# Performance work log

Measured on AMD Instinct MI355X. Metric: run time of the kernel, lower is better.

The kernel has to match this reference:

```python
import jax, jax.numpy as jnp
import numpy as np

MARGIN = 0.5
N_CLASSES = 100

def setup_inputs() -> dict:
    key = jax.random.key(0)
    k1, k2 = jax.random.split(key)
    n, d = 8192, 128
    inputs = jax.random.normal(k1, (n, d), dtype=jnp.float32)
    targets = jax.random.randint(k2, (n,), 0, N_CLASSES, dtype=jnp.int64)
    return {"inputs": inputs, "targets": targets}

def reference(inputs, targets):
    # pairwise squared euclidean distances: [n, n]
    sq = jnp.sum(inputs * inputs, axis=1)  # [n]
    dist = sq[:, None] + sq[None, :] - 2.0 * (inputs @ inputs.T)
    dist = jnp.maximum(dist, 0.0)
    # positive mask: same label (diagonal included, matching original)
    mask = targets[:, None] == targets[None, :]  # [n, n] bool
    big = jnp.float32(1e30)
    dist_ap = jnp.max(jnp.where(mask, dist, -big), axis=1)  # hardest positive per row
    dist_an = jnp.min(jnp.where(mask, big, dist), axis=1)   # hardest negative per row
    loss = jnp.sum(jax.nn.relu(dist_ap - dist_an + MARGIN))
    return loss
```

## Files before the change

kernel.cpp:

```cpp
#include <hip/hip_runtime.h>
#include <hip/hip_bf16.h>

#define D 128
#define MARGIN 0.5f
#define NSPLIT 16
#define NCHUNK 32

typedef __attribute__((ext_vector_type(8))) short bf16x8;
typedef __attribute__((ext_vector_type(4))) float f32x4;

__global__ void prep_kernel(const float* __restrict__ x,
                            float* __restrict__ sq,
                            unsigned* __restrict__ ap,
                            unsigned* __restrict__ an,
                            __hip_bfloat16* __restrict__ xb,
                            float* __restrict__ out, int n) {
    int tid = threadIdx.x;
    int row = blockIdx.x * 4 + (tid >> 6);
    int lane = tid & 63;
    const float2* xr = (const float2*)(x + (size_t)row * D);
    float2 v = xr[lane];
    __hip_bfloat162 b2;
    b2.x = __float2bfloat16(v.x);
    b2.y = __float2bfloat16(v.y);
    ((__hip_bfloat162*)(xb + (size_t)row * D))[lane] = b2;
    float s = v.x * v.x + v.y * v.y;
    #pragma unroll
    for (int o = 32; o > 0; o >>= 1) s += __shfl_xor(s, o, 64);
    if (lane == 0) {
        sq[row] = s;
        ap[row] = 0u;
        an[row] = 0x7F800000u;
    }
    if (blockIdx.x == 0 && tid == 0) *out = 0.0f;
}

__launch_bounds__(256, 2)
__global__ void gram_kernel(const __hip_bfloat16* __restrict__ xb,
                            const float* __restrict__ sq,
                            const int* __restrict__ tgt,
                            unsigned* __restrict__ ap,
                            unsigned* __restrict__ an, int n) {
    const int tid  = threadIdx.x;
    const int wid  = tid >> 6;
    const int lane = tid & 63;
    const int quad = lane >> 4;
    const int l    = lane & 15;
    const int gw     = blockIdx.x * 4 + wid;
    const int istrip = gw >> 4;
    const int jsplit = gw & 15;
    const int i0 = istrip * 64;
    const int j0 = jsplit * (16 * NCHUNK);

    bf16x8 afrag[4][4];
    {
        const __hip_bfloat16* abase = xb + (size_t)(i0 + l) * D + quad * 8;
        #pragma unroll
        for (int mt = 0; mt < 4; ++mt)
            #pragma unroll
            for (int ks = 0; ks < 4; ++ks)
                afrag[mt][ks] = *(const bf16x8*)(abase + (size_t)mt * 16 * D + ks * 32);
    }

    int li[4][4];
    #pragma unroll
    for (int mt = 0; mt < 4; ++mt)
        #pragma unroll
        for (int reg = 0; reg < 4; ++reg)
            li[mt][reg] = tgt[i0 + mt * 16 + quad * 4 + reg];

    float lap[16], lan[16];
    #pragma unroll
    for (int k = 0; k < 16; ++k) { lap[k] = -1e30f; lan[k] = 1e30f; }

    const __hip_bfloat16* bbase = xb + (size_t)(j0 + l) * D + quad * 8;

    bf16x8 bf[2][4];
    float  sj[2];
    int    tj[2];

    #define LOADB(buf, c)                                                   \
        do {                                                                \
            const __hip_bfloat16* p_ = bbase + (size_t)(c) * 16 * D;        \
            bf[buf][0] = *(const bf16x8*)(p_);                              \
            bf[buf][1] = *(const bf16x8*)(p_ + 32);                         \
            bf[buf][2] = *(const bf16x8*)(p_ + 64);                         \
            bf[buf][3] = *(const bf16x8*)(p_ + 96);                         \
            sj[buf] = sq[j0 + (c) * 16 + l];                                \
            tj[buf] = tgt[j0 + (c) * 16 + l];                               \
        } while (0)

    #define COMPUTE(buf)                                                    \
        do {                                                                \
            f32x4 acc[4];                                                   \
            _Pragma("unroll")                                               \
            for (int mt = 0; mt < 4; ++mt) acc[mt] = (f32x4){0.f,0.f,0.f,0.f}; \
            _Pragma("unroll")                                               \
            for (int ks = 0; ks < 4; ++ks)                                  \
                _Pragma("unroll")                                           \
                for (int mt = 0; mt < 4; ++mt)                              \
                    acc[mt] = __builtin_amdgcn_mfma_f32_16x16x32_bf16(      \
                        afrag[mt][ks], bf[buf][ks], acc[mt], 0, 0, 0);      \
            float sjc = sj[buf]; int tjc = tj[buf];                         \
            _Pragma("unroll")                                               \
            for (int mt = 0; mt < 4; ++mt)                                  \
                _Pragma("unroll")                                           \
                for (int reg = 0; reg < 4; ++reg) {                         \
                    float t = fmaf(-2.0f, acc[mt][reg], sjc);               \
                    bool same = (li[mt][reg] == tjc);                       \
                    lap[mt*4+reg] = fmaxf(lap[mt*4+reg], same ? t : -1e30f);\
                    lan[mt*4+reg] = fminf(lan[mt*4+reg], same ? 1e30f : t); \
                }                                                           \
        } while (0)

    LOADB(0, 0);
    for (int c = 0; c < NCHUNK; c += 2) {
        LOADB(1, c + 1);
        COMPUTE(0);
        if (c < NCHUNK - 2) LOADB(0, c + 2);
        COMPUTE(1);
    }
    #undef LOADB
    #undef COMPUTE

    #pragma unroll
    for (int mt = 0; mt < 4; ++mt)
        #pragma unroll
        for (int reg = 0; reg < 4; ++reg) {
            float p = lap[mt*4+reg], q = lan[mt*4+reg];
            #pragma unroll
            for (int o = 1; o < 16; o <<= 1) {
                p = fmaxf(p, __shfl_xor(p, o, 64));
                q = fminf(q, __shfl_xor(q, o, 64));
            }
            if (l == mt * 4 + reg) {
                int gi = i0 + mt * 16 + quad * 4 + reg;
                float s = sq[gi];
                atomicMax(&ap[gi], __float_as_uint(fmaxf(s + p, 0.0f)));
                atomicMin(&an[gi], __float_as_uint(fmaxf(s + q, 0.0f)));
            }
        }
}

__global__ void final_kernel(const unsigned* __restrict__ ap,
                             const unsigned* __restrict__ an,
                             float* __restrict__ out, int n) {
    int i = blockIdx.x * blockDim.x + threadIdx.x;
    float v = 0.f;
    if (i < n) {
        float p = __uint_as_float(ap[i]);
        float q = __uint_as_float(an[i]);
        v = fmaxf(p - q + MARGIN, 0.0f);
    }
    #pragma unroll
    for (int o = 32; o > 0; o >>= 1) v += __shfl_xor(v, o, 64);
    __shared__ float ws[4];
    int lane = threadIdx.x & 63, w = threadIdx.x >> 6;
    if (lane == 0) ws[w] = v;
    __syncthreads();
    if (threadIdx.x == 0) atomicAdd(out, ws[0] + ws[1] + ws[2] + ws[3]);
}

extern "C" void kernel_launch(void* const* d_in, const int* in_sizes, int n_in,
                              void* d_out, int out_size, void* d_ws, size_t ws_size,
                              hipStream_t stream) {
    const float* x   = (const float*)d_in[0];
    const int*   tgt = (const int*)d_in[1];
    float* out = (float*)d_out;
    const int n = in_sizes[1];

    float*          sq = (float*)d_ws;
    unsigned*       ap = (unsigned*)((char*)d_ws + (size_t)n * 4);
    unsigned*       an = ap + n;
    __hip_bfloat16* xb = (__hip_bfloat16*)((char*)d_ws + (size_t)n * 12);

    prep_kernel<<<n / 4, 256, 0, stream>>>(x, sq, ap, an, xb, out, n);
    gram_kernel<<<(n / 64) * NSPLIT / 4, 256, 0, stream>>>(xb, sq, tgt, ap, an, n);
    final_kernel<<<n / 256, 256, 0, stream>>>(ap, an, out, n);
}
```

Baseline: 103.1 us.

## Stage shared B tiles in LDS with swizzle and double buffering

Before, each wave streamed its own B fragments straight from global memory, covering 64 rows over a private j range. Now a block of 4 waves covers 128 rows and shares each 64-row B tile, staged in swizzled double-buffered LDS with register prefetch. This raises B reuse across waves and lowers global traffic, and each wave now holds 32 rows, so register pressure falls enough to allow 4 blocks per CU. The cost is a __syncthreads per tile and LDS read traffic, and each wave does fewer MFMAs per B fragment.

```diff
diff --git a/kernel.cpp b/kernel.cpp
--- a/kernel.cpp
+++ b/kernel.cpp
@@ -4,7 +4,6 @@
 #define D 128
 #define MARGIN 0.5f
 #define NSPLIT 16
-#define NCHUNK 32
 
 typedef __attribute__((ext_vector_type(8))) short bf16x8;
 typedef __attribute__((ext_vector_type(4))) float f32x4;
@@ -35,106 +34,126 @@
     if (blockIdx.x == 0 && tid == 0) *out = 0.0f;
 }
 
-__launch_bounds__(256, 2)
+__launch_bounds__(256, 4)
 __global__ void gram_kernel(const __hip_bfloat16* __restrict__ xb,
                             const float* __restrict__ sq,
                             const int* __restrict__ tgt,
                             unsigned* __restrict__ ap,
                             unsigned* __restrict__ an, int n) {
+    __shared__ __align__(16) __hip_bfloat16 Bs[2][64 * D];
+
     const int tid  = threadIdx.x;
     const int wid  = tid >> 6;
     const int lane = tid & 63;
     const int quad = lane >> 4;
     const int l    = lane & 15;
-    const int gw     = blockIdx.x * 4 + wid;
-    const int istrip = gw >> 4;
-    const int jsplit = gw & 15;
-    const int i0 = istrip * 64;
-    const int j0 = jsplit * (16 * NCHUNK);
-
-    bf16x8 afrag[4][4];
+    const int i0   = blockIdx.x * 128;
+    const int jspan = n / NSPLIT;
+    const int njit  = jspan / 64;
+    const int j0    = blockIdx.y * jspan;
+    const int rowbase = i0 + wid * 32;
+
+    bf16x8 afrag[2][4];
     {
-        const __hip_bfloat16* abase = xb + (size_t)(i0 + l) * D + quad * 8;
-        #pragma unroll
-        for (int mt = 0; mt < 4; ++mt)
+        const __hip_bfloat16* abase = xb + (size_t)(rowbase + l) * D + quad * 8;
+        #pragma unroll
+        for (int mt = 0; mt < 2; ++mt)
             #pragma unroll
             for (int ks = 0; ks < 4; ++ks)
                 afrag[mt][ks] = *(const bf16x8*)(abase + (size_t)mt * 16 * D + ks * 32);
     }
 
-    int li[4][4];
-    #pragma unroll
-    for (int mt = 0; mt < 4; ++mt)
+    int li[2][4];
+    #pragma unroll
+    for (int mt = 0; mt < 2; ++mt)
         #pragma unroll
         for (int reg = 0; reg < 4; ++reg)
-            li[mt][reg] = tgt[i0 + mt * 16 + quad * 4 + reg];
-
-    float lap[16], lan[16];
-    #pragma unroll
-    for (int k = 0; k < 16; ++k) { lap[k] = -1e30f; lan[k] = 1e30f; }
-
-    const __hip_bfloat16* bbase = xb + (size_t)(j0 + l) * D + quad * 8;
-
-    bf16x8 bf[2][4];
-    float  sj[2];
-    int    tj[2];
-
-    #define LOADB(buf, c)                                                   \
-        do {                                                                \
-            const __hip_bfloat16* p_ = bbase + (size_t)(c) * 16 * D;        \
-            bf[buf][0] = *(const bf16x8*)(p_);                              \
-            bf[buf][1] = *(const bf16x8*)(p_ + 32);                         \
-            bf[buf][2] = *(const bf16x8*)(p_ + 64);                         \
-            bf[buf][3] = *(const bf16x8*)(p_ + 96);                         \
-            sj[buf] = sq[j0 + (c) * 16 + l];                                \
-            tj[buf] = tgt[j0 + (c) * 16 + l];                               \
+            li[mt][reg] = tgt[rowbase + mt * 16 + quad * 4 + reg];
+
+    float lap[8], lan[8];
+    #pragma unroll
+    for (int k = 0; k < 8; ++k) { lap[k] = -1e30f; lan[k] = 1e30f; }
+
+    const int q0 = wid * 256;
+    float4 streg[4];
+    const char* xbb = (const char*)xb;
+
+    #define LOADTILE(jt0)                                                     \
+        do {                                                                  \
+            _Pragma("unroll")                                                 \
+            for (int i_ = 0; i_ < 4; ++i_) {                                  \
+                int q_ = q0 + i_ * 64 + lane;                                 \
+                int r_ = q_ >> 4;                                             \
+                int c_ = (q_ & 15) ^ (r_ & 15);                               \
+                streg[i_] = *(const float4*)(xbb + (size_t)((jt0) + r_) * 256 \
+                                                 + (size_t)c_ * 16);          \
+            }                                                                 \
         } while (0)
 
-    #define COMPUTE(buf)                                                    \
-        do {                                                                \
-            f32x4 acc[4];                                                   \
-            _Pragma("unroll")                                               \
-            for (int mt = 0; mt < 4; ++mt) acc[mt] = (f32x4){0.f,0.f,0.f,0.f}; \
-            _Pragma("unroll")                                               \
-            for (int ks = 0; ks < 4; ++ks)                                  \
-                _Pragma("unroll")                                           \
-                for (int mt = 0; mt < 4; ++mt)                              \
-                    acc[mt] = __builtin_amdgcn_mfma_f32_16x16x32_bf16(      \
-                        afrag[mt][ks], bf[buf][ks], acc[mt], 0, 0, 0);      \
-            float sjc = sj[buf]; int tjc = tj[buf];                         \
-            _Pragma("unroll")                                               \
-            for (int mt = 0; mt < 4; ++mt)                                  \
-                _Pragma("unroll")                                           \
-                for (int reg = 0; reg < 4; ++reg) {                         \
-                    float t = fmaf(-2.0f, acc[mt][reg], sjc);               \
-                    bool same = (li[mt][reg] == tjc);                       \
-                    lap[mt*4+reg] = fmaxf(lap[mt*4+reg], same ? t : -1e30f);\
-                    lan[mt*4+reg] = fminf(lan[mt*4+reg], same ? 1e30f : t); \
-                }                                                           \
+    #define WRITETILE(buf)                                                    \
+        do {                                                                  \
+            char* b_ = (char*)&Bs[buf][0];                                    \
+            _Pragma("unroll")                                                 \
+            for (int i_ = 0; i_ < 4; ++i_) {                                  \
+                int q_ = q0 + i_ * 64 + lane;                                 \
+                *(float4*)(b_ + (size_t)q_ * 16) = streg[i_];                 \
+            }                                                                 \
         } while (0)
 
-    LOADB(0, 0);
-    for (int c = 0; c < NCHUNK; c += 2) {
-        LOADB(1, c + 1);
-        COMPUTE(0);
-        if (c < NCHUNK - 2) LOADB(0, c + 2);
-        COMPUTE(1);
-    }
-    #undef LOADB
-    #undef COMPUTE
-
-    #pragma unroll
-    for (int mt = 0; mt < 4; ++mt)
+    LOADTILE(j0);
+    WRITETILE(0);
+    __syncthreads();
+
+    for (int jj = 0; jj < njit; ++jj) {
+        const int cur = jj & 1;
+        if (jj < njit - 1) LOADTILE(j0 + (jj + 1) * 64);
+
+        const char* Bb = (const char*)&Bs[cur][0];
+        const int jbase = j0 + jj * 64;
+        #pragma unroll
+        for (int jt = 0; jt < 4; ++jt) {
+            f32x4 acc0 = (f32x4){0.f, 0.f, 0.f, 0.f};
+            f32x4 acc1 = (f32x4){0.f, 0.f, 0.f, 0.f};
+            #pragma unroll
+            for (int ks = 0; ks < 4; ++ks) {
+                int q = (jt * 16 + l) * 16 + ((ks * 4 + quad) ^ l);
+                bf16x8 bfr = *(const bf16x8*)(Bb + (size_t)q * 16);
+                acc0 = __builtin_amdgcn_mfma_f32_16x16x32_bf16(afrag[0][ks], bfr, acc0, 0, 0, 0);
+                acc1 = __builtin_amdgcn_mfma_f32_16x16x32_bf16(afrag[1][ks], bfr, acc1, 0, 0, 0);
+            }
+            float sjc = sq[jbase + jt * 16 + l];
+            int   tjc = tgt[jbase + jt * 16 + l];
+            #pragma unroll
+            for (int reg = 0; reg < 4; ++reg) {
+                float t0 = fmaf(-2.0f, acc0[reg], sjc);
+                float t1 = fmaf(-2.0f, acc1[reg], sjc);
+                bool s0 = (li[0][reg] == tjc);
+                bool s1 = (li[1][reg] == tjc);
+                lap[reg]     = fmaxf(lap[reg],     s0 ? t0 : -1e30f);
+                lan[reg]     = fminf(lan[reg],     s0 ? 1e30f : t0);
+                lap[4 + reg] = fmaxf(lap[4 + reg], s1 ? t1 : -1e30f);
+                lan[4 + reg] = fminf(lan[4 + reg], s1 ? 1e30f : t1);
+            }
+        }
+
+        if (jj < njit - 1) WRITETILE(cur ^ 1);
+        __syncthreads();
+    }
+    #undef LOADTILE
+    #undef WRITETILE
+
+    #pragma unroll
+    for (int mt = 0; mt < 2; ++mt)
         #pragma unroll
         for (int reg = 0; reg < 4; ++reg) {
-            float p = lap[mt*4+reg], q = lan[mt*4+reg];
+            float p = lap[mt * 4 + reg], q = lan[mt * 4 + reg];
             #pragma unroll
             for (int o = 1; o < 16; o <<= 1) {
                 p = fmaxf(p, __shfl_xor(p, o, 64));
                 q = fminf(q, __shfl_xor(q, o, 64));
             }
             if (l == mt * 4 + reg) {
-                int gi = i0 + mt * 16 + quad * 4 + reg;
+                int gi = rowbase + mt * 16 + quad * 4 + reg;
                 float s = sq[gi];
                 atomicMax(&ap[gi], __float_as_uint(fmaxf(s + p, 0.0f)));
                 atomicMin(&an[gi], __float_as_uint(fmaxf(s + q, 0.0f)));
@@ -175,6 +194,7 @@
     __hip_bfloat16* xb = (__hip_bfloat16*)((char*)d_ws + (size_t)n * 12);
 
     prep_kernel<<<n / 4, 256, 0, stream>>>(x, sq, ap, an, xb, out, n);
-    gram_kernel<<<(n / 64) * NSPLIT / 4, 256, 0, stream>>>(xb, sq, tgt, ap, an, n);
+    dim3 grid(n / 128, NSPLIT);
+    gram_kernel<<<grid, 256, 0, stream>>>(xb, sq, tgt, ap, an, n);
     final_kernel<<<n / 256, 256, 0, stream>>>(ap, an, out, n);
 }
```

Result: slower. 112.9 us (+9.6%).
